# Performance work log

Measured on AMD Instinct MI355X. Metric: run time of the kernel, lower is better.

Reference implementation:

```python
import jax, jax.numpy as jnp
from jax import lax
import numpy as np

V, H = 512, 512


def gru_cell(x, h, Wih, Whh, bih, bhh):
    # PyTorch GRUCell: r,z,n gate order
    gi = x @ Wih.T + bih
    gh = h @ Whh.T + bhh
    ir, iz, inn = jnp.split(gi, 3, axis=-1)
    hr, hz, hn = jnp.split(gh, 3, axis=-1)
    r = jax.nn.sigmoid(ir + hr)
    z = jax.nn.sigmoid(iz + hz)
    n = jnp.tanh(inn + r * hn)
    return (1.0 - z) * n + z * h


def setup_inputs() -> dict:
    key = jax.random.key(0)
    ks = jax.random.split(key, 20)
    S, T, B = 200, 200, 256
    w = lambda k, shape: (jax.random.normal(k, shape, jnp.float32) * 0.05)
    inp = {
        "input_seq": jax.random.randint(ks[0], (S, B), 0, V),
        "input_len": jax.random.randint(ks[1], (B,), 1, S + 1),
        "target_seq": jax.random.randint(ks[2], (T, B), 0, V),
        "enc_embed": w(ks[3], (V, H)),
        "enc_Wih": w(ks[4], (3 * H, H)),
        "enc_Whh": w(ks[5], (3 * H, H)),
        "enc_bih": w(ks[6], (3 * H,)),
        "enc_bhh": w(ks[7], (3 * H,)),
        "att_W": w(ks[8], (H, H)),
        "att_b": w(ks[9], (H,)),
        "dec_embed": w(ks[10], (V, H)),
        "dec_Wih": w(ks[11], (3 * H, H)),
        "dec_Whh": w(ks[12], (3 * H, H)),
        "dec_bih": w(ks[13], (3 * H,)),
        "dec_bhh": w(ks[14], (3 * H,)),
        "mlp_W": w(ks[15], (H, 2 * H)),
        "mlp_b": w(ks[16], (H,)),
        "out_W": w(ks[17], (V, H)),
        "out_b": w(ks[18], (V,)),
    }
    return inp


def reference(input_seq, input_len, target_seq, enc_embed, enc_Wih, enc_Whh,
              enc_bih, enc_bhh, att_W, att_b, dec_embed, dec_Wih, dec_Whh,
              dec_bih, dec_bhh, mlp_W, mlp_b, out_W, out_b):
    S, B = input_seq.shape
    T = target_seq.shape[0]

    # ---- Encoder: length-masked GRU (equivalent to pack/pad) ----
    xs = enc_embed[input_seq]                              # (S,B,H)
    mask = jnp.arange(S)[:, None] < input_len[None, :]     # (S,B)
    h0 = jnp.zeros((B, H), xs.dtype)

    def estep(h, inp):
        x, m = inp
        m = m[:, None]
        hn = gru_cell(x, h, enc_Wih, enc_Whh, enc_bih, enc_bhh)
        h = jnp.where(m, hn, h)
        return h, jnp.where(m, h, 0.0)                     # padded outputs are zero

    h_enc, enc_out = lax.scan(estep, h0, (xs, mask))       # h_enc (B,H), enc_out (S,B,H)

    # ---- Decoder: teacher forcing (training path) ----
    dec_tokens = jnp.concatenate(
        [jnp.ones((1, B), target_seq.dtype), target_seq[:-1]], axis=0)  # start token 1
    dec_emb = dec_embed[dec_tokens]                        # (T,B,H)

    def dstep(h, emb_t):
        ah = jax.nn.relu(h @ att_W.T + att_b)              # (B,H)
        e = jnp.einsum('sbh,bh->bs', enc_out, ah)          # additive-style score
        att = jax.nn.softmax(e, axis=1)                    # (B,S)
        ctx = jnp.einsum('sbh,bs->bh', enc_out, att)       # (B,H)
        x = jnp.tanh(jnp.concatenate([emb_t, ctx], axis=1) @ mlp_W.T + mlp_b)
        hn = gru_cell(x, h, dec_Wih, dec_Whh, dec_bih, dec_bhh)
        dist = jax.nn.softmax(hn @ out_W.T + out_b, axis=1)
        return hn, dist

    _, dists = lax.scan(dstep, h_enc, dec_emb)             # (T,B,V)

    # ---- Loss: -log p[target] with clamp (== cal_loss) ----
    p = jnp.maximum(dists, 1e-10)
    tgt_p = jnp.take_along_axis(p, target_seq[:, :, None], axis=2)[..., 0]
    loss = jnp.mean(-jnp.log(tgt_p))

    # ---- Accuracy ----
    inference = jnp.argmax(dists, axis=-1)                 # (T,B)
    temacc = (inference == target_seq).astype(jnp.float32)
    all_acc = jnp.mean(temacc)
    acc = jnp.mean((jnp.sum(1.0 - temacc, axis=0) == 0).astype(jnp.float32))
    return inference.astype(jnp.float32), loss, acc, all_acc
```

## Files before the change

kernel.cpp:

```cpp
#include <hip/hip_runtime.h>
#include <math.h>

#define B 256
#define Hh 512
#define S 200
#define T 200
#define VOC 512
#define G3 1536
#define PAD 36

struct d4 { double x, y, z, w; };
__device__ __forceinline__ d4 tod4(const float4 a) {
    d4 r; r.x = a.x; r.y = a.y; r.z = a.z; r.w = a.w; return r;
}
__device__ __forceinline__ double dotd(const d4& a, const d4& b) {
    return a.x * b.x + a.y * b.y + a.z * b.z + a.w * b.w;
}
__device__ __forceinline__ double sigd(double x) { return 1.0 / (1.0 + exp(-x)); }

__global__ __launch_bounds__(256) void gemm_at(
    const float* __restrict__ A,
    const float* __restrict__ W, int ldw, int woff,
    const float* __restrict__ bias,
    float* __restrict__ C, int ldc)
{
    __shared__ float As[32][PAD];
    __shared__ float Ws[32][PAD];
    const int tid = threadIdx.x;
    const int tx = tid & 15, ty = tid >> 4;
    const int j0 = blockIdx.x * 32, m0 = blockIdx.y * 32;
    const int lr = tid >> 3, lc = (tid & 7) * 4;

    double acc00 = 0.0, acc01 = 0.0, acc10 = 0.0, acc11 = 0.0;

    for (int k0 = 0; k0 < 512; k0 += 32) {
        float4 av = *(const float4*)(A + (size_t)(m0 + lr) * 512 + k0 + lc);
        float4 wv = *(const float4*)(W + (size_t)(j0 + lr) * ldw + woff + k0 + lc);
        __syncthreads();
        *(float4*)&As[lr][lc] = av;
        *(float4*)&Ws[lr][lc] = wv;
        __syncthreads();
#pragma unroll
        for (int kk = 0; kk < 32; kk += 4) {
            d4 a0 = tod4(*(const float4*)&As[ty][kk]);
            d4 a1 = tod4(*(const float4*)&As[ty + 16][kk]);
            d4 b0 = tod4(*(const float4*)&Ws[tx][kk]);
            d4 b1 = tod4(*(const float4*)&Ws[tx + 16][kk]);
            acc00 += dotd(a0, b0);
            acc01 += dotd(a0, b1);
            acc10 += dotd(a1, b0);
            acc11 += dotd(a1, b1);
        }
    }
    const int ms[2] = { m0 + ty, m0 + ty + 16 };
    const int js[2] = { j0 + tx, j0 + tx + 16 };
    double accs[2][2] = { { acc00, acc01 }, { acc10, acc11 } };
#pragma unroll
    for (int mi = 0; mi < 2; ++mi)
#pragma unroll
        for (int ji = 0; ji < 2; ++ji) {
            int m = ms[mi], j = js[ji];
            C[(size_t)m * ldc + j] = (float)(accs[mi][ji] + (double)bias[j]);
        }
}

__global__ __launch_bounds__(512) void enc_step(
    const float* __restrict__ h_in, float* __restrict__ h_out,
    const float* __restrict__ gi_tab, const int* __restrict__ iseq,
    const int* __restrict__ ilen, const float* __restrict__ Whh,
    const float* __restrict__ bhh, int s, float* __restrict__ enc_out)
{
    __shared__ float Hs[32][68];
    __shared__ float Ws[48][68];
    const int tid = threadIdx.x;
    const int j_l = tid & 15, b_l = tid >> 4;
    const int j0 = blockIdx.x * 16, b0 = blockIdx.y * 32;
    const int j = j0 + j_l, b = b0 + b_l;

    int ml = 0;
    for (int i = 0; i < 32; ++i) ml = max(ml, ilen[b0 + i]);
    if (s >= ml) {
        h_out[(size_t)b * 512 + j] = h_in[(size_t)b * 512 + j];
        enc_out[((size_t)s * B + b) * 512 + j] = 0.f;
        return;
    }

    double ar = 0.0, az = 0.0, an = 0.0;
    for (int kt = 0; kt < 512; kt += 64) {
        __syncthreads();
        {
            int row = tid >> 4, c4 = (tid & 15) * 4;
            *(float4*)&Hs[row][c4] =
                *(const float4*)(h_in + (size_t)(b0 + row) * 512 + kt + c4);
            for (int idx = tid; idx < 768; idx += 512) {
                int r = idx >> 4, cc = (idx & 15) * 4;
                int g = r >> 4, jj = r & 15;
                *(float4*)&Ws[r][cc] =
                    *(const float4*)(Whh + (size_t)(g * 512 + j0 + jj) * 512 + kt + cc);
            }
        }
        __syncthreads();
#pragma unroll
        for (int kk = 0; kk < 64; kk += 4) {
            d4 hv = tod4(*(const float4*)&Hs[b_l][kk]);
            ar += dotd(hv, tod4(*(const float4*)&Ws[j_l][kk]));
            az += dotd(hv, tod4(*(const float4*)&Ws[16 + j_l][kk]));
            an += dotd(hv, tod4(*(const float4*)&Ws[32 + j_l][kk]));
        }
    }

    float hold = h_in[(size_t)b * 512 + j];
    float hnew = hold;
    if (s < ilen[b]) {
        int tok = iseq[s * B + b];
        const float* gi = gi_tab + (size_t)tok * G3;
        double r = sigd((double)gi[j] + ar + (double)bhh[j]);
        double z = sigd((double)gi[512 + j] + az + (double)bhh[512 + j]);
        double n = tanh((double)gi[1024 + j] + r * (an + (double)bhh[1024 + j]));
        hnew = (float)((1.0 - z) * n + z * (double)hold);
        enc_out[((size_t)s * B + b) * 512 + j] = hnew;
    } else {
        enc_out[((size_t)s * B + b) * 512 + j] = 0.f;
    }
    h_out[(size_t)b * 512 + j] = hnew;
}

__global__ __launch_bounds__(512) void proj(
    const float* __restrict__ h,
    const float* __restrict__ att_W, const float* __restrict__ att_b,
    const float* __restrict__ out_W, const float* __restrict__ out_b,
    float* __restrict__ ah, float* __restrict__ logits, int t)
{
    __shared__ float As[32][68];
    __shared__ float Ws[32][68];
    const int tid = threadIdx.x;
    const int tx = tid & 15, ty = tid >> 4;
    const int R0 = blockIdx.x * 32, m0 = blockIdx.y * 32;
    const bool is_att = (R0 < 512);
    if (is_att && t >= T) return;

    double a0 = 0.0, a1 = 0.0;
    for (int kt = 0; kt < 512; kt += 64) {
        __syncthreads();
        {
            int row = tid >> 4, c4 = (tid & 15) * 4;
            *(float4*)&As[row][c4] =
                *(const float4*)(h + (size_t)(m0 + row) * 512 + kt + c4);
            int R = R0 + row;
            const float* ws = is_att ? (att_W + (size_t)R * 512)
                                     : (out_W + (size_t)(R - 512) * 512);
            *(float4*)&Ws[row][c4] = *(const float4*)(ws + kt + c4);
        }
        __syncthreads();
#pragma unroll
        for (int kk = 0; kk < 64; kk += 4) {
            d4 av = tod4(*(const float4*)&As[ty][kk]);
            a0 += dotd(av, tod4(*(const float4*)&Ws[tx][kk]));
            a1 += dotd(av, tod4(*(const float4*)&Ws[16 + tx][kk]));
        }
    }

    const int m = m0 + ty;
    const int Ra = R0 + tx, Rb = R0 + tx + 16;
    if (is_att) {
        double v0 = a0 + (double)att_b[Ra]; if (v0 < 0.0) v0 = 0.0;
        double v1 = a1 + (double)att_b[Rb]; if (v1 < 0.0) v1 = 0.0;
        ah[(size_t)m * 512 + Ra] = (float)v0;
        ah[(size_t)m * 512 + Rb] = (float)v1;
    } else {
        logits[(size_t)m * 512 + (Ra - 512)] = (float)(a0 + (double)out_b[Ra - 512]);
        logits[(size_t)m * 512 + (Rb - 512)] = (float)(a1 + (double)out_b[Rb - 512]);
    }
}

__global__ __launch_bounds__(256) void attn_x_softmax(
    const float* __restrict__ enc_out, const float* __restrict__ ah,
    const float* __restrict__ mlp_W, const float* __restrict__ mlp_tab,
    const int* __restrict__ input_len, const int* __restrict__ target_seq,
    const float* __restrict__ logits, int t,
    float* __restrict__ xbuf, float* __restrict__ nll,
    float* __restrict__ inference)
{
    const int bid = blockIdx.x, tid = threadIdx.x;

    if (bid < B) {
        if (t >= T) return;
        __shared__ float scx[4][512];
        __shared__ double sml[8];
        __shared__ float ctxl[512];
        const int b = bid;
        const int wave = tid >> 6, lane = tid & 63;
        const int len = input_len[b];
        const float* ahb = ah + (size_t)b * 512;
        d4 aa1 = tod4(*(const float4*)(ahb + lane * 4));
        d4 aa2 = tod4(*(const float4*)(ahb + 256 + lane * 4));
        double m = -INFINITY, l = 0.0;
        d4 c1 = {0,0,0,0}, c2 = {0,0,0,0};
        for (int s = wave; s < len; s += 4) {
            const float* row = enc_out + ((size_t)s * B + b) * 512;
            d4 e1 = tod4(*(const float4*)(row + lane * 4));
            d4 e2 = tod4(*(const float4*)(row + 256 + lane * 4));
            double p = dotd(e1, aa1) + dotd(e2, aa2);
#pragma unroll
            for (int off = 32; off >= 1; off >>= 1) p += __shfl_xor(p, off, 64);
            double mn = fmax(m, p);
            double sc = (m == mn) ? 1.0 : exp(m - mn);
            double w = exp(p - mn);
            l = l * sc + w;
            c1.x = c1.x * sc + w * e1.x; c1.y = c1.y * sc + w * e1.y;
            c1.z = c1.z * sc + w * e1.z; c1.w = c1.w * sc + w * e1.w;
            c2.x = c2.x * sc + w * e2.x; c2.y = c2.y * sc + w * e2.y;
            c2.z = c2.z * sc + w * e2.z; c2.w = c2.w * sc + w * e2.w;
            m = mn;
        }
        if (lane == 0) { sml[wave] = m; sml[4 + wave] = l; }
        *(float4*)&scx[wave][lane * 4] =
            make_float4((float)c1.x, (float)c1.y, (float)c1.z, (float)c1.w);
        *(float4*)&scx[wave][256 + lane * 4] =
            make_float4((float)c2.x, (float)c2.y, (float)c2.z, (float)c2.w);
        __syncthreads();
        double M = fmax(fmax(sml[0], sml[1]), fmax(sml[2], sml[3]));
        if (len < S) M = fmax(M, 0.0);
        double w0 = exp(sml[0] - M), w1x = exp(sml[1] - M);
        double w2x = exp(sml[2] - M), w3 = exp(sml[3] - M);
        double L = sml[4] * w0 + sml[5] * w1x + sml[6] * w2x + sml[7] * w3
                 + (double)(S - len) * exp(0.0 - M);
        for (int jj = tid; jj < 512; jj += 256) {
            double v = (double)scx[0][jj] * w0 + (double)scx[1][jj] * w1x
                     + (double)scx[2][jj] * w2x + (double)scx[3][jj] * w3;
            ctxl[jj] = (float)(v / L);
        }
        __syncthreads();

        const int tok = (t == 0) ? 1 : target_seq[(t - 1) * B + b];
        const int q = tid & 3;
        const int rbase = tid >> 2;
#pragma unroll
        for (int pass = 0; pass < 8; ++pass) {
            const int jr = pass * 64 + rbase;
            const float* wr = mlp_W + (size_t)jr * 1024 + 512;
            double a = 0.0;
            for (int k = q * 4; k < 512; k += 16) {
                a += dotd(tod4(*(const float4*)&ctxl[k]),
                          tod4(*(const float4*)(wr + k)));
            }
            a += __shfl_xor(a, 1, 64);
            a += __shfl_xor(a, 2, 64);
            if (q == 0)
                xbuf[(size_t)b * 512 + jr] =
                    (float)tanh((double)mlp_tab[(size_t)tok * 512 + jr] + a);
        }
    } else {
        if (t < 1) return;
        __shared__ float red_f[256];
        __shared__ double red_d[256];
        __shared__ int red_i[256];
        const int sb = bid - B;
        const float* lg = logits + (size_t)sb * 512;
        const float l0 = lg[tid], l1 = lg[256 + tid];
        red_f[tid] = fmaxf(l0, l1);
        __syncthreads();
        for (int off = 128; off > 0; off >>= 1) {
            if (tid < off) red_f[tid] = fmaxf(red_f[tid], red_f[tid + off]);
            __syncthreads();
        }
        const double mx = (double)red_f[0];
        __syncthreads();
        const double e0 = exp((double)l0 - mx), e1 = exp((double)l1 - mx);
        red_d[tid] = e0 + e1;
        __syncthreads();
        for (int off = 128; off > 0; off >>= 1) {
            if (tid < off) red_d[tid] += red_d[tid + off];
            __syncthreads();
        }
        const double Z = red_d[0];
        __syncthreads();
        const float p0 = (float)(e0 / Z), p1 = (float)(e1 / Z);
        float v; int idx;
        if (p0 >= p1) { v = p0; idx = tid; } else { v = p1; idx = 256 + tid; }
        red_f[tid] = v; red_i[tid] = idx;
        __syncthreads();
        for (int off = 128; off > 0; off >>= 1) {
            if (tid < off) {
                float ov = red_f[tid + off]; int oi = red_i[tid + off];
                if (ov > red_f[tid] || (ov == red_f[tid] && oi < red_i[tid])) {
                    red_f[tid] = ov; red_i[tid] = oi;
                }
            }
            __syncthreads();
        }
        if (tid == 0) {
            int tg = target_seq[(t - 1) * B + sb];
            float pt = (float)(exp((double)lg[tg] - mx) / Z);
            pt = fmaxf(pt, 1e-10f);
            nll[(t - 1) * B + sb] = (float)(-log((double)pt));
            inference[(t - 1) * B + sb] = (float)red_i[0];
        }
    }
}

__global__ __launch_bounds__(256) void dec_gru(
    const float* __restrict__ x, const float* __restrict__ h_in,
    const float* __restrict__ Wih, const float* __restrict__ Whh,
    const float* __restrict__ bih, const float* __restrict__ bhh,
    float* __restrict__ h_out)
{
    __shared__ float Xs[16][36];
    __shared__ float Hs2[16][36];
    __shared__ float Wi[48][36];
    __shared__ float Wh[48][36];
    const int tid = threadIdx.x;
    const int j_l = tid & 15, b_l = tid >> 4;
    const int j0 = blockIdx.x * 16, b0 = blockIdx.y * 16;
    const int j = j0 + j_l, b = b0 + b_l;

    double air = 0, aiz = 0, ain = 0, ahr = 0, ahz = 0, ahn = 0;
    for (int kt = 0; kt < 512; kt += 32) {
        __syncthreads();
        for (int idx = tid; idx < 1024; idx += 256) {
            if (idx < 128) {
                int row = idx >> 3, c4 = (idx & 7) * 4;
                *(float4*)&Xs[row][c4] =
                    *(const float4*)(x + (size_t)(b0 + row) * 512 + kt + c4);
            } else if (idx < 256) {
                int w = idx - 128; int row = w >> 3, c4 = (w & 7) * 4;
                *(float4*)&Hs2[row][c4] =
                    *(const float4*)(h_in + (size_t)(b0 + row) * 512 + kt + c4);
            } else if (idx < 640) {
                int w = idx - 256; int row = w >> 3, c4 = (w & 7) * 4;
                int g = row >> 4, jj = row & 15;
                *(float4*)&Wi[row][c4] =
                    *(const float4*)(Wih + (size_t)(g * 512 + j0 + jj) * 512 + kt + c4);
            } else {
                int w = idx - 640; int row = w >> 3, c4 = (w & 7) * 4;
                int g = row >> 4, jj = row & 15;
                *(float4*)&Wh[row][c4] =
                    *(const float4*)(Whh + (size_t)(g * 512 + j0 + jj) * 512 + kt + c4);
            }
        }
        __syncthreads();
#pragma unroll
        for (int kk = 0; kk < 32; kk += 4) {
            d4 xv = tod4(*(const float4*)&Xs[b_l][kk]);
            d4 hv = tod4(*(const float4*)&Hs2[b_l][kk]);
            air += dotd(xv, tod4(*(const float4*)&Wi[j_l][kk]));
            aiz += dotd(xv, tod4(*(const float4*)&Wi[16 + j_l][kk]));
            ain += dotd(xv, tod4(*(const float4*)&Wi[32 + j_l][kk]));
            ahr += dotd(hv, tod4(*(const float4*)&Wh[j_l][kk]));
            ahz += dotd(hv, tod4(*(const float4*)&Wh[16 + j_l][kk]));
            ahn += dotd(hv, tod4(*(const float4*)&Wh[32 + j_l][kk]));
        }
    }

    double r = sigd(air + (double)bih[j] + ahr + (double)bhh[j]);
    double z = sigd(aiz + (double)bih[512 + j] + ahz + (double)bhh[512 + j]);
    double n = tanh(ain + (double)bih[1024 + j] + r * (ahn + (double)bhh[1024 + j]));
    float hold = h_in[(size_t)b * 512 + j];
    h_out[(size_t)b * 512 + j] = (float)((1.0 - z) * n + z * (double)hold);
}

__global__ __launch_bounds__(256) void finalize_k(
    const float* __restrict__ nll, const float* __restrict__ inference,
    const int* __restrict__ target, float* __restrict__ out3)
{
    const int tid = threadIdx.x;
    int wrong = 0;
    double match = 0.0;
    const int b = tid;
    for (int t = 0; t < T; ++t) {
        float inf = inference[t * B + b];
        float tg = (float)target[t * B + b];
        bool ok = (inf == tg);
        match += ok ? 1.0 : 0.0;
        wrong |= !ok;
    }
    double lsum = 0.0;
    for (int i = tid; i < T * B; i += 256) lsum += (double)nll[i];

    __shared__ double sl[256], sm_[256], sa[256];
    sl[tid] = lsum; sm_[tid] = match; sa[tid] = wrong ? 0.0 : 1.0;
    __syncthreads();
    for (int off = 128; off > 0; off >>= 1) {
        if (tid < off) {
            sl[tid] += sl[tid + off];
            sm_[tid] += sm_[tid + off];
            sa[tid] += sa[tid + off];
        }
        __syncthreads();
    }
    if (tid == 0) {
        out3[0] = (float)(sl[0] / (double)(T * B));
        out3[1] = (float)(sa[0] / (double)B);
        out3[2] = (float)(sm_[0] / (double)(T * B));
    }
}

extern "C" void kernel_launch(void* const* d_in, const int* in_sizes, int n_in,
                              void* d_out, int out_size, void* d_ws, size_t ws_size,
                              hipStream_t stream)
{
    const int*   input_seq  = (const int*)d_in[0];
    const int*   input_len  = (const int*)d_in[1];
    const int*   target_seq = (const int*)d_in[2];
    const float* enc_embed  = (const float*)d_in[3];
    const float* enc_Wih    = (const float*)d_in[4];
    const float* enc_Whh    = (const float*)d_in[5];
    const float* enc_bih    = (const float*)d_in[6];
    const float* enc_bhh    = (const float*)d_in[7];
    const float* att_W      = (const float*)d_in[8];
    const float* att_b      = (const float*)d_in[9];
    const float* dec_embed  = (const float*)d_in[10];
    const float* dec_Wih    = (const float*)d_in[11];
    const float* dec_Whh    = (const float*)d_in[12];
    const float* dec_bih    = (const float*)d_in[13];
    const float* dec_bhh    = (const float*)d_in[14];
    const float* mlp_W      = (const float*)d_in[15];
    const float* mlp_b      = (const float*)d_in[16];
    const float* out_W      = (const float*)d_in[17];
    const float* out_b      = (const float*)d_in[18];

    float* out = (float*)d_out;

    float* gi_tab  = (float*)d_ws;
    float* mlp_tab = gi_tab + (size_t)VOC * G3;
    float* h0      = mlp_tab + (size_t)VOC * Hh;
    float* h1      = h0 + (size_t)B * Hh;
    float* ahb     = h1 + (size_t)B * Hh;
    float* xb      = ahb + (size_t)B * Hh;
    float* lgb     = xb + (size_t)B * Hh;
    float* nllb    = lgb + (size_t)B * Hh;
    float* enc_out = nllb + (size_t)T * B;

    hipMemsetAsync(h0, 0, (size_t)B * Hh * sizeof(float), stream);

    gemm_at<<<dim3(48, 16), 256, 0, stream>>>(
        enc_embed, enc_Wih, 512, 0, enc_bih, gi_tab, G3);
    gemm_at<<<dim3(16, 16), 256, 0, stream>>>(
        dec_embed, mlp_W, 1024, 0, mlp_b, mlp_tab, Hh);

    for (int s = 0; s < S; ++s) {
        const float* hc = (s & 1) ? h1 : h0;
        float* hx = (s & 1) ? h0 : h1;
        enc_step<<<dim3(32, 8), 512, 0, stream>>>(
            hc, hx, gi_tab, input_seq, input_len, enc_Whh, enc_bhh, s, enc_out);
    }

    for (int t = 0; t <= T; ++t) {
        const float* hc = (t & 1) ? h1 : h0;
        float* hx = (t & 1) ? h0 : h1;
        proj<<<dim3(32, 8), 512, 0, stream>>>(
            hc, att_W, att_b, out_W, out_b, ahb, lgb, t);
        attn_x_softmax<<<dim3(2 * B), 256, 0, stream>>>(
            enc_out, ahb, mlp_W, mlp_tab, input_len, target_seq,
            lgb, t, xb, nllb, out);
        if (t < T) {
            dec_gru<<<dim3(32, 16), 256, 0, stream>>>(
                xb, hc, dec_Wih, dec_Whh, dec_bih, dec_bhh, hx);
        }
    }

    finalize_k<<<dim3(1), 256, 0, stream>>>(nllb, out, target_seq, out + (size_t)T * B);
}
```

Baseline: 33.33 ms.

## Move recurrent GEMMs to FP64 MFMA kernels with separate elementwise combine

Replaces the scalar double-precision dot-product kernels for the encoder step, projection and decoder GRU with a shared gemm64 kernel. It uses the 16x16x4 f64 MFMA instruction, probes the lane layout at runtime, and prefetches weight tiles through registers. The GEMM writes double partial sums to a workspace, and small combine kernels then apply biases and the gate nonlinearities. This should cut the per-step FP64 ALU cost, at the price of twice as many launches per step and an extra round trip of double intermediates through global memory.

```diff
diff --git a/kernel.cpp b/kernel.cpp
--- a/kernel.cpp
+++ b/kernel.cpp
@@ -17,6 +17,12 @@
     return a.x * b.x + a.y * b.y + a.z * b.z + a.w * b.w;
 }
 __device__ __forceinline__ double sigd(double x) { return 1.0 / (1.0 + exp(-x)); }
+
+typedef double f64x4 __attribute__((ext_vector_type(4)));
+
+__device__ __forceinline__ unsigned long long dbits(double v) {
+    return (unsigned long long)__double_as_longlong(v);
+}
 
 __global__ __launch_bounds__(256) void gemm_at(
     const float* __restrict__ A,
@@ -64,56 +70,123 @@
         }
 }
 
-__global__ __launch_bounds__(512) void enc_step(
+__global__ __launch_bounds__(128) void gemm64(
+    const float* __restrict__ A0, const float* __restrict__ A1,
+    const float* __restrict__ W0, const float* __restrict__ W1,
+    int split, int N, double* __restrict__ Csum,
+    const int* __restrict__ ilen, int s)
+{
+    const int n0 = blockIdx.x * 64;
+    const int m0 = blockIdx.y * 16;
+    if (ilen) {
+        int ml = 0;
+        for (int i = 0; i < 16; ++i) ml = max(ml, ilen[m0 + i]);
+        if (s >= ml) return;
+    }
+    __shared__ float As[16][516];
+    __shared__ float Ws[64][68];
+    const int tid = threadIdx.x;
+    const bool lo = (n0 < split);
+    const float* Ab = lo ? A0 : A1;
+    const float* Wb = lo ? W0 : W1;
+    const int nw = lo ? n0 : (n0 - split);
+
+    const int lane = tid & 63;
+    const int wv = tid >> 6;
+    const int lr = lane & 15;
+    const int g  = lane >> 4;
+
+    f64x4 zf = { 0.0, 0.0, 0.0, 0.0 };
+    f64x4 va = __builtin_amdgcn_mfma_f64_16x16x4f64(
+        (double)(1ULL << lane), 1.0, zf, 0, 0, 0);
+    const unsigned long long MM = 0xFFFFFFFFFFFFFULL;
+    const unsigned long long M0 = (1ULL << 36) | (1ULL << 20) | (1ULL << 4);
+    const int fam0 = __all(
+        ((dbits(va[0]) & MM) == M0) && ((dbits(va[1]) & MM) == M0) &&
+        ((dbits(va[2]) & MM) == M0) && ((dbits(va[3]) & MM) == M0));
+    const int am = fam0 ? (lane & 15) : (lane >> 2);
+    const int ak = fam0 ? (lane >> 4) : (lane & 3);
+    f64x4 vr = __builtin_amdgcn_mfma_f64_16x16x4f64(
+        (double)(1ULL << am), 1.0, zf, 0, 0, 0);
+
+#pragma unroll 4
+    for (int i = 0; i < 16; ++i) {
+        *(float4*)&As[i][tid * 4] =
+            *(const float4*)(Ab + (size_t)(m0 + i) * 512 + tid * 4);
+    }
+
+    float4 wreg[8];
+#pragma unroll
+    for (int i = 0; i < 8; ++i) {
+        int x4 = i * 128 + tid, row = x4 >> 4, c4 = (x4 & 15) * 4;
+        wreg[i] = *(const float4*)(Wb + (size_t)(nw + row) * 512 + c4);
+    }
+    __syncthreads();
+#pragma unroll
+    for (int i = 0; i < 8; ++i) {
+        int x4 = i * 128 + tid, row = x4 >> 4, c4 = (x4 & 15) * 4;
+        *(float4*)&Ws[row][c4] = wreg[i];
+    }
+    __syncthreads();
+
+    const int nl0 = wv * 32;
+    f64x4 c0 = { 0.0, 0.0, 0.0, 0.0 };
+    f64x4 c1 = { 0.0, 0.0, 0.0, 0.0 };
+
+    for (int k0 = 0; k0 < 512; k0 += 64) {
+        const bool more = (k0 + 64) < 512;
+        if (more) {
+#pragma unroll
+            for (int i = 0; i < 8; ++i) {
+                int x4 = i * 128 + tid, row = x4 >> 4, c4 = (x4 & 15) * 4;
+                wreg[i] = *(const float4*)(Wb + (size_t)(nw + row) * 512
+                                           + k0 + 64 + c4);
+            }
+        }
+#pragma unroll
+        for (int kk = 0; kk < 16; ++kk) {
+            double a  = (double)As[am][k0 + kk * 4 + ak];
+            double b0 = (double)Ws[nl0 + lr][kk * 4 + g];
+            double b1 = (double)Ws[nl0 + 16 + lr][kk * 4 + g];
+            c0 = __builtin_amdgcn_mfma_f64_16x16x4f64(a, b0, c0, 0, 0, 0);
+            c1 = __builtin_amdgcn_mfma_f64_16x16x4f64(a, b1, c1, 0, 0, 0);
+        }
+        __syncthreads();
+        if (more) {
+#pragma unroll
+            for (int i = 0; i < 8; ++i) {
+                int x4 = i * 128 + tid, row = x4 >> 4, c4 = (x4 & 15) * 4;
+                *(float4*)&Ws[row][c4] = wreg[i];
+            }
+            __syncthreads();
+        }
+    }
+
+#pragma unroll
+    for (int d = 0; d < 4; ++d) {
+        const int rowd = (int)((dbits(vr[d]) >> 52) & 0x7ff) - 1025;
+        const size_t m = (size_t)(m0 + rowd);
+        Csum[m * N + n0 + nl0 + lr]      = c0[d];
+        Csum[m * N + n0 + nl0 + 16 + lr] = c1[d];
+    }
+}
+
+__global__ __launch_bounds__(256) void enc_combine(
+    const double* __restrict__ Csum,
     const float* __restrict__ h_in, float* __restrict__ h_out,
     const float* __restrict__ gi_tab, const int* __restrict__ iseq,
-    const int* __restrict__ ilen, const float* __restrict__ Whh,
-    const float* __restrict__ bhh, int s, float* __restrict__ enc_out)
-{
-    __shared__ float Hs[32][68];
-    __shared__ float Ws[48][68];
-    const int tid = threadIdx.x;
-    const int j_l = tid & 15, b_l = tid >> 4;
-    const int j0 = blockIdx.x * 16, b0 = blockIdx.y * 32;
-    const int j = j0 + j_l, b = b0 + b_l;
-
-    int ml = 0;
-    for (int i = 0; i < 32; ++i) ml = max(ml, ilen[b0 + i]);
-    if (s >= ml) {
-        h_out[(size_t)b * 512 + j] = h_in[(size_t)b * 512 + j];
-        enc_out[((size_t)s * B + b) * 512 + j] = 0.f;
-        return;
-    }
-
-    double ar = 0.0, az = 0.0, an = 0.0;
-    for (int kt = 0; kt < 512; kt += 64) {
-        __syncthreads();
-        {
-            int row = tid >> 4, c4 = (tid & 15) * 4;
-            *(float4*)&Hs[row][c4] =
-                *(const float4*)(h_in + (size_t)(b0 + row) * 512 + kt + c4);
-            for (int idx = tid; idx < 768; idx += 512) {
-                int r = idx >> 4, cc = (idx & 15) * 4;
-                int g = r >> 4, jj = r & 15;
-                *(float4*)&Ws[r][cc] =
-                    *(const float4*)(Whh + (size_t)(g * 512 + j0 + jj) * 512 + kt + cc);
-            }
-        }
-        __syncthreads();
-#pragma unroll
-        for (int kk = 0; kk < 64; kk += 4) {
-            d4 hv = tod4(*(const float4*)&Hs[b_l][kk]);
-            ar += dotd(hv, tod4(*(const float4*)&Ws[j_l][kk]));
-            az += dotd(hv, tod4(*(const float4*)&Ws[16 + j_l][kk]));
-            an += dotd(hv, tod4(*(const float4*)&Ws[32 + j_l][kk]));
-        }
-    }
-
-    float hold = h_in[(size_t)b * 512 + j];
+    const int* __restrict__ ilen, const float* __restrict__ bhh,
+    int s, float* __restrict__ enc_out)
+{
+    const int idx = blockIdx.x * 256 + threadIdx.x;
+    const int b = idx >> 9, j = idx & 511;
+    const float hold = h_in[idx];
     float hnew = hold;
     if (s < ilen[b]) {
-        int tok = iseq[s * B + b];
+        const int tok = iseq[s * B + b];
         const float* gi = gi_tab + (size_t)tok * G3;
+        const double* Cb = Csum + (size_t)b * 1536;
+        double ar = Cb[j], az = Cb[512 + j], an = Cb[1024 + j];
         double r = sigd((double)gi[j] + ar + (double)bhh[j]);
         double z = sigd((double)gi[512 + j] + az + (double)bhh[512 + j]);
         double n = tanh((double)gi[1024 + j] + r * (an + (double)bhh[1024 + j]));
@@ -122,55 +195,41 @@
     } else {
         enc_out[((size_t)s * B + b) * 512 + j] = 0.f;
     }
-    h_out[(size_t)b * 512 + j] = hnew;
-}
-
-__global__ __launch_bounds__(512) void proj(
-    const float* __restrict__ h,
-    const float* __restrict__ att_W, const float* __restrict__ att_b,
-    const float* __restrict__ out_W, const float* __restrict__ out_b,
+    h_out[idx] = hnew;
+}
+
+__global__ __launch_bounds__(256) void proj_combine(
+    const double* __restrict__ Csum,
+    const float* __restrict__ att_b, const float* __restrict__ out_b,
     float* __restrict__ ah, float* __restrict__ logits, int t)
 {
-    __shared__ float As[32][68];
-    __shared__ float Ws[32][68];
-    const int tid = threadIdx.x;
-    const int tx = tid & 15, ty = tid >> 4;
-    const int R0 = blockIdx.x * 32, m0 = blockIdx.y * 32;
-    const bool is_att = (R0 < 512);
-    if (is_att && t >= T) return;
-
-    double a0 = 0.0, a1 = 0.0;
-    for (int kt = 0; kt < 512; kt += 64) {
-        __syncthreads();
-        {
-            int row = tid >> 4, c4 = (tid & 15) * 4;
-            *(float4*)&As[row][c4] =
-                *(const float4*)(h + (size_t)(m0 + row) * 512 + kt + c4);
-            int R = R0 + row;
-            const float* ws = is_att ? (att_W + (size_t)R * 512)
-                                     : (out_W + (size_t)(R - 512) * 512);
-            *(float4*)&Ws[row][c4] = *(const float4*)(ws + kt + c4);
-        }
-        __syncthreads();
-#pragma unroll
-        for (int kk = 0; kk < 64; kk += 4) {
-            d4 av = tod4(*(const float4*)&As[ty][kk]);
-            a0 += dotd(av, tod4(*(const float4*)&Ws[tx][kk]));
-            a1 += dotd(av, tod4(*(const float4*)&Ws[16 + tx][kk]));
-        }
-    }
-
-    const int m = m0 + ty;
-    const int Ra = R0 + tx, Rb = R0 + tx + 16;
-    if (is_att) {
-        double v0 = a0 + (double)att_b[Ra]; if (v0 < 0.0) v0 = 0.0;
-        double v1 = a1 + (double)att_b[Rb]; if (v1 < 0.0) v1 = 0.0;
-        ah[(size_t)m * 512 + Ra] = (float)v0;
-        ah[(size_t)m * 512 + Rb] = (float)v1;
+    const int idx = blockIdx.x * 256 + threadIdx.x;
+    const int m = idx >> 10, n = idx & 1023;
+    const double v = Csum[idx];
+    if (n < 512) {
+        if (t >= T) return;
+        double r = v + (double)att_b[n]; if (r < 0.0) r = 0.0;
+        ah[(size_t)m * 512 + n] = (float)r;
     } else {
-        logits[(size_t)m * 512 + (Ra - 512)] = (float)(a0 + (double)out_b[Ra - 512]);
-        logits[(size_t)m * 512 + (Rb - 512)] = (float)(a1 + (double)out_b[Rb - 512]);
-    }
+        logits[(size_t)m * 512 + (n - 512)] = (float)(v + (double)out_b[n - 512]);
+    }
+}
+
+__global__ __launch_bounds__(256) void dec_combine(
+    const double* __restrict__ Csum,
+    const float* __restrict__ bih, const float* __restrict__ bhh,
+    const float* __restrict__ h_in, float* __restrict__ h_out)
+{
+    const int idx = blockIdx.x * 256 + threadIdx.x;
+    const int b = idx >> 9, j = idx & 511;
+    const double* Cb = Csum + (size_t)b * 3072;
+    double air = Cb[j],        aiz = Cb[512 + j],  ain = Cb[1024 + j];
+    double ahr = Cb[1536 + j], ahz = Cb[2048 + j], ahn = Cb[2560 + j];
+    double r = sigd(air + (double)bih[j] + ahr + (double)bhh[j]);
+    double z = sigd(aiz + (double)bih[512 + j] + ahz + (double)bhh[512 + j]);
+    double n = tanh(ain + (double)bih[1024 + j] + r * (ahn + (double)bhh[1024 + j]));
+    const float hold = h_in[idx];
+    h_out[idx] = (float)((1.0 - z) * n + z * (double)hold);
 }
 
 __global__ __launch_bounds__(256) void attn_x_softmax(
@@ -297,66 +356,6 @@
             inference[(t - 1) * B + sb] = (float)red_i[0];
         }
     }
-}
-
-__global__ __launch_bounds__(256) void dec_gru(
-    const float* __restrict__ x, const float* __restrict__ h_in,
-    const float* __restrict__ Wih, const float* __restrict__ Whh,
-    const float* __restrict__ bih, const float* __restrict__ bhh,
-    float* __restrict__ h_out)
-{
-    __shared__ float Xs[16][36];
-    __shared__ float Hs2[16][36];
-    __shared__ float Wi[48][36];
-    __shared__ float Wh[48][36];
-    const int tid = threadIdx.x;
-    const int j_l = tid & 15, b_l = tid >> 4;
-    const int j0 = blockIdx.x * 16, b0 = blockIdx.y * 16;
-    const int j = j0 + j_l, b = b0 + b_l;
-
-    double air = 0, aiz = 0, ain = 0, ahr = 0, ahz = 0, ahn = 0;
-    for (int kt = 0; kt < 512; kt += 32) {
-        __syncthreads();
-        for (int idx = tid; idx < 1024; idx += 256) {
-            if (idx < 128) {
-                int row = idx >> 3, c4 = (idx & 7) * 4;
-                *(float4*)&Xs[row][c4] =
-                    *(const float4*)(x + (size_t)(b0 + row) * 512 + kt + c4);
-            } else if (idx < 256) {
-                int w = idx - 128; int row = w >> 3, c4 = (w & 7) * 4;
-                *(float4*)&Hs2[row][c4] =
-                    *(const float4*)(h_in + (size_t)(b0 + row) * 512 + kt + c4);
-            } else if (idx < 640) {
-                int w = idx - 256; int row = w >> 3, c4 = (w & 7) * 4;
-                int g = row >> 4, jj = row & 15;
-                *(float4*)&Wi[row][c4] =
-                    *(const float4*)(Wih + (size_t)(g * 512 + j0 + jj) * 512 + kt + c4);
-            } else {
-                int w = idx - 640; int row = w >> 3, c4 = (w & 7) * 4;
-                int g = row >> 4, jj = row & 15;
-                *(float4*)&Wh[row][c4] =
-                    *(const float4*)(Whh + (size_t)(g * 512 + j0 + jj) * 512 + kt + c4);
-            }
-        }
-        __syncthreads();
-#pragma unroll
-        for (int kk = 0; kk < 32; kk += 4) {
-            d4 xv = tod4(*(const float4*)&Xs[b_l][kk]);
-            d4 hv = tod4(*(const float4*)&Hs2[b_l][kk]);
-            air += dotd(xv, tod4(*(const float4*)&Wi[j_l][kk]));
-            aiz += dotd(xv, tod4(*(const float4*)&Wi[16 + j_l][kk]));
-            ain += dotd(xv, tod4(*(const float4*)&Wi[32 + j_l][kk]));
-            ahr += dotd(hv, tod4(*(const float4*)&Wh[j_l][kk]));
-            ahz += dotd(hv, tod4(*(const float4*)&Wh[16 + j_l][kk]));
-            ahn += dotd(hv, tod4(*(const float4*)&Wh[32 + j_l][kk]));
-        }
-    }
-
-    double r = sigd(air + (double)bih[j] + ahr + (double)bhh[j]);
-    double z = sigd(aiz + (double)bih[512 + j] + ahz + (double)bhh[512 + j]);
-    double n = tanh(ain + (double)bih[1024 + j] + r * (ahn + (double)bhh[1024 + j]));
-    float hold = h_in[(size_t)b * 512 + j];
-    h_out[(size_t)b * 512 + j] = (float)((1.0 - z) * n + z * (double)hold);
 }
 
 __global__ __launch_bounds__(256) void finalize_k(
@@ -430,6 +429,7 @@
     float* lgb     = xb + (size_t)B * Hh;
     float* nllb    = lgb + (size_t)B * Hh;
     float* enc_out = nllb + (size_t)T * B;
+    double* gsum   = (double*)(enc_out + (size_t)S * B * Hh);
 
     hipMemsetAsync(h0, 0, (size_t)B * Hh * sizeof(float), stream);
 
@@ -441,21 +441,27 @@
     for (int s = 0; s < S; ++s) {
         const float* hc = (s & 1) ? h1 : h0;
         float* hx = (s & 1) ? h0 : h1;
-        enc_step<<<dim3(32, 8), 512, 0, stream>>>(
-            hc, hx, gi_tab, input_seq, input_len, enc_Whh, enc_bhh, s, enc_out);
+        gemm64<<<dim3(24, 16), 128, 0, stream>>>(
+            hc, hc, enc_Whh, enc_Whh, 1536, 1536, gsum, input_len, s);
+        enc_combine<<<dim3(512), 256, 0, stream>>>(
+            gsum, hc, hx, gi_tab, input_seq, input_len, enc_bhh, s, enc_out);
     }
 
     for (int t = 0; t <= T; ++t) {
         const float* hc = (t & 1) ? h1 : h0;
         float* hx = (t & 1) ? h0 : h1;
-        proj<<<dim3(32, 8), 512, 0, stream>>>(
-            hc, att_W, att_b, out_W, out_b, ahb, lgb, t);
+        gemm64<<<dim3(16, 16), 128, 0, stream>>>(
+            hc, hc, att_W, out_W, 512, 1024, gsum, nullptr, 0);
+        proj_combine<<<dim3(1024), 256, 0, stream>>>(
+            gsum, att_b, out_b, ahb, lgb, t);
         attn_x_softmax<<<dim3(2 * B), 256, 0, stream>>>(
             enc_out, ahb, mlp_W, mlp_tab, input_len, target_seq,
             lgb, t, xb, nllb, out);
         if (t < T) {
-            dec_gru<<<dim3(32, 16), 256, 0, stream>>>(
-                xb, hc, dec_Wih, dec_Whh, dec_bih, dec_bhh, hx);
+            gemm64<<<dim3(48, 16), 128, 0, stream>>>(
+                xb, hc, dec_Wih, dec_Whh, 1536, 3072, gsum, nullptr, 0);
+            dec_combine<<<dim3(512), 256, 0, stream>>>(
+                gsum, dec_bih, dec_bhh, hc, hx);
         }
     }
 
```

Result: no change. 33.51 ms (+0.6%).

## Split attention into two-pass softmax context and separate tiled ctx-MLP GEMM

Applied to the files above, without the earlier changes.

The fused per-batch attention kernel, which did an online softmax and then a per-row matvec against mlp_W, is split in two. The first kernel stores scores in shared memory, does a block max and sum, and accumulates the context in a second pass over enc_out. A new shared-memory tiled GEMM then computes the ctx part of the MLP for all batches at once. This lets mlp_W be reused across batch rows instead of being reread by each of 256 blocks, at the cost of an extra launch, a second read of enc_out and a serial single-thread sum.

```diff
diff --git a/kernel.cpp b/kernel.cpp
--- a/kernel.cpp
+++ b/kernel.cpp
@@ -173,29 +173,26 @@
     }
 }
 
-__global__ __launch_bounds__(256) void attn_x_softmax(
+__global__ __launch_bounds__(256) void attn_ctx(
     const float* __restrict__ enc_out, const float* __restrict__ ah,
-    const float* __restrict__ mlp_W, const float* __restrict__ mlp_tab,
     const int* __restrict__ input_len, const int* __restrict__ target_seq,
     const float* __restrict__ logits, int t,
-    float* __restrict__ xbuf, float* __restrict__ nll,
+    float* __restrict__ ctxb, float* __restrict__ nll,
     float* __restrict__ inference)
 {
     const int bid = blockIdx.x, tid = threadIdx.x;
 
     if (bid < B) {
         if (t >= T) return;
-        __shared__ float scx[4][512];
-        __shared__ double sml[8];
-        __shared__ float ctxl[512];
+        __shared__ double e_w[200];
+        __shared__ double red[256];
         const int b = bid;
         const int wave = tid >> 6, lane = tid & 63;
         const int len = input_len[b];
         const float* ahb = ah + (size_t)b * 512;
         d4 aa1 = tod4(*(const float4*)(ahb + lane * 4));
         d4 aa2 = tod4(*(const float4*)(ahb + 256 + lane * 4));
-        double m = -INFINITY, l = 0.0;
-        d4 c1 = {0,0,0,0}, c2 = {0,0,0,0};
+
         for (int s = wave; s < len; s += 4) {
             const float* row = enc_out + ((size_t)s * B + b) * 512;
             d4 e1 = tod4(*(const float4*)(row + lane * 4));
@@ -203,53 +200,43 @@
             double p = dotd(e1, aa1) + dotd(e2, aa2);
 #pragma unroll
             for (int off = 32; off >= 1; off >>= 1) p += __shfl_xor(p, off, 64);
-            double mn = fmax(m, p);
-            double sc = (m == mn) ? 1.0 : exp(m - mn);
-            double w = exp(p - mn);
-            l = l * sc + w;
-            c1.x = c1.x * sc + w * e1.x; c1.y = c1.y * sc + w * e1.y;
-            c1.z = c1.z * sc + w * e1.z; c1.w = c1.w * sc + w * e1.w;
-            c2.x = c2.x * sc + w * e2.x; c2.y = c2.y * sc + w * e2.y;
-            c2.z = c2.z * sc + w * e2.z; c2.w = c2.w * sc + w * e2.w;
-            m = mn;
-        }
-        if (lane == 0) { sml[wave] = m; sml[4 + wave] = l; }
-        *(float4*)&scx[wave][lane * 4] =
-            make_float4((float)c1.x, (float)c1.y, (float)c1.z, (float)c1.w);
-        *(float4*)&scx[wave][256 + lane * 4] =
-            make_float4((float)c2.x, (float)c2.y, (float)c2.z, (float)c2.w);
-        __syncthreads();
-        double M = fmax(fmax(sml[0], sml[1]), fmax(sml[2], sml[3]));
+            if (lane == 0) e_w[s] = p;
+        }
+        __syncthreads();
+
+        double mloc = -INFINITY;
+        for (int s2 = tid; s2 < len; s2 += 256) mloc = fmax(mloc, e_w[s2]);
+        red[tid] = mloc;
+        __syncthreads();
+        for (int off = 128; off > 0; off >>= 1) {
+            if (tid < off) red[tid] = fmax(red[tid], red[tid + off]);
+            __syncthreads();
+        }
+        double M = red[0];
         if (len < S) M = fmax(M, 0.0);
-        double w0 = exp(sml[0] - M), w1x = exp(sml[1] - M);
-        double w2x = exp(sml[2] - M), w3 = exp(sml[3] - M);
-        double L = sml[4] * w0 + sml[5] * w1x + sml[6] * w2x + sml[7] * w3
-                 + (double)(S - len) * exp(0.0 - M);
-        for (int jj = tid; jj < 512; jj += 256) {
-            double v = (double)scx[0][jj] * w0 + (double)scx[1][jj] * w1x
-                     + (double)scx[2][jj] * w2x + (double)scx[3][jj] * w3;
-            ctxl[jj] = (float)(v / L);
-        }
-        __syncthreads();
-
-        const int tok = (t == 0) ? 1 : target_seq[(t - 1) * B + b];
-        const int q = tid & 3;
-        const int rbase = tid >> 2;
-#pragma unroll
-        for (int pass = 0; pass < 8; ++pass) {
-            const int jr = pass * 64 + rbase;
-            const float* wr = mlp_W + (size_t)jr * 1024 + 512;
-            double a = 0.0;
-            for (int k = q * 4; k < 512; k += 16) {
-                a += dotd(tod4(*(const float4*)&ctxl[k]),
-                          tod4(*(const float4*)(wr + k)));
-            }
-            a += __shfl_xor(a, 1, 64);
-            a += __shfl_xor(a, 2, 64);
-            if (q == 0)
-                xbuf[(size_t)b * 512 + jr] =
-                    (float)tanh((double)mlp_tab[(size_t)tok * 512 + jr] + a);
-        }
+        __syncthreads();
+
+        if (tid < len) e_w[tid] = exp(e_w[tid] - M);
+        __syncthreads();
+
+        if (tid == 0) {
+            double acc = 0.0;
+            for (int s2 = 0; s2 < len; ++s2) acc += e_w[s2];
+            acc += (double)(S - len) * exp(0.0 - M);
+            red[0] = acc;
+        }
+        __syncthreads();
+        const double L = red[0];
+
+        double acc0 = 0.0, acc1 = 0.0;
+        for (int s2 = 0; s2 < len; ++s2) {
+            const float* row = enc_out + ((size_t)s2 * B + b) * 512;
+            const double w = e_w[s2];
+            acc0 += w * (double)row[tid];
+            acc1 += w * (double)row[tid + 256];
+        }
+        ctxb[(size_t)b * 512 + tid]       = (float)(acc0 / L);
+        ctxb[(size_t)b * 512 + tid + 256] = (float)(acc1 / L);
     } else {
         if (t < 1) return;
         __shared__ float red_f[256];
@@ -297,6 +284,45 @@
             inference[(t - 1) * B + sb] = (float)red_i[0];
         }
     }
+}
+
+__global__ __launch_bounds__(512) void xgemm(
+    const float* __restrict__ ctxb, const float* __restrict__ mlp_W,
+    const float* __restrict__ mlp_tab, const int* __restrict__ target_seq,
+    int t, float* __restrict__ xb)
+{
+    __shared__ float As[32][68];
+    __shared__ float Ws[32][68];
+    const int tid = threadIdx.x;
+    const int tx = tid & 15, ty = tid >> 4;
+    const int j0 = blockIdx.x * 32, m0 = blockIdx.y * 32;
+
+    double a0 = 0.0, a1 = 0.0;
+    for (int kt = 0; kt < 512; kt += 64) {
+        __syncthreads();
+        {
+            int row = tid >> 4, c4 = (tid & 15) * 4;
+            *(float4*)&As[row][c4] =
+                *(const float4*)(ctxb + (size_t)(m0 + row) * 512 + kt + c4);
+            *(float4*)&Ws[row][c4] =
+                *(const float4*)(mlp_W + (size_t)(j0 + row) * 1024 + 512 + kt + c4);
+        }
+        __syncthreads();
+#pragma unroll
+        for (int kk = 0; kk < 64; kk += 4) {
+            d4 av = tod4(*(const float4*)&As[ty][kk]);
+            a0 += dotd(av, tod4(*(const float4*)&Ws[tx][kk]));
+            a1 += dotd(av, tod4(*(const float4*)&Ws[16 + tx][kk]));
+        }
+    }
+
+    const int m = m0 + ty;
+    const int tok = (t == 0) ? 1 : target_seq[(t - 1) * B + m];
+    const int ja = j0 + tx, jb = j0 + tx + 16;
+    xb[(size_t)m * 512 + ja] =
+        (float)tanh((double)mlp_tab[(size_t)tok * 512 + ja] + a0);
+    xb[(size_t)m * 512 + jb] =
+        (float)tanh((double)mlp_tab[(size_t)tok * 512 + jb] + a1);
 }
 
 __global__ __launch_bounds__(256) void dec_gru(
@@ -430,6 +456,7 @@
     float* lgb     = xb + (size_t)B * Hh;
     float* nllb    = lgb + (size_t)B * Hh;
     float* enc_out = nllb + (size_t)T * B;
+    float* ctxb    = enc_out + (size_t)S * B * Hh;
 
     hipMemsetAsync(h0, 0, (size_t)B * Hh * sizeof(float), stream);
 
@@ -450,10 +477,11 @@
         float* hx = (t & 1) ? h0 : h1;
         proj<<<dim3(32, 8), 512, 0, stream>>>(
             hc, att_W, att_b, out_W, out_b, ahb, lgb, t);
-        attn_x_softmax<<<dim3(2 * B), 256, 0, stream>>>(
-            enc_out, ahb, mlp_W, mlp_tab, input_len, target_seq,
-            lgb, t, xb, nllb, out);
+        attn_ctx<<<dim3(2 * B), 256, 0, stream>>>(
+            enc_out, ahb, input_len, target_seq, lgb, t, ctxb, nllb, out);
         if (t < T) {
+            xgemm<<<dim3(16, 8), 512, 0, stream>>>(
+                ctxb, mlp_W, mlp_tab, target_seq, t, xb);
             dec_gru<<<dim3(32, 16), 256, 0, stream>>>(
                 xb, hc, dec_Wih, dec_Whh, dec_bih, dec_bhh, hx);
         }
```

New measurement: 34.87 ms. +4.6%, slower.

## Register-prefetch next K tile and shrink tiles in GRU and projection kernels

Applied to the files above, without the earlier changes.

Rewrites the encoder step, projection, and decoder GRU kernels to prefetch the next 64-wide K tile into registers while computing on the current shared-memory tile. Tiles shrink to 16x16 with 256-thread blocks, giving more blocks per launch (e.g. 512 for the encoder and 1024 for the projection). The decoder GRU K tile grows from 32 to 64. The aim is to hide global-load latency and raise occupancy on these latency-bound per-timestep launches, at the cost of more register pressure and less reuse per block.

```diff
diff --git a/kernel.cpp b/kernel.cpp
--- a/kernel.cpp
+++ b/kernel.cpp
@@ -64,42 +64,59 @@
         }
 }
 
-__global__ __launch_bounds__(512) void enc_step(
+__global__ __launch_bounds__(256) void enc_step2(
     const float* __restrict__ h_in, float* __restrict__ h_out,
     const float* __restrict__ gi_tab, const int* __restrict__ iseq,
     const int* __restrict__ ilen, const float* __restrict__ Whh,
     const float* __restrict__ bhh, int s, float* __restrict__ enc_out)
 {
-    __shared__ float Hs[32][68];
+    __shared__ float Hs[16][68];
     __shared__ float Ws[48][68];
     const int tid = threadIdx.x;
     const int j_l = tid & 15, b_l = tid >> 4;
-    const int j0 = blockIdx.x * 16, b0 = blockIdx.y * 32;
+    const int j0 = blockIdx.x * 16, b0 = blockIdx.y * 16;
     const int j = j0 + j_l, b = b0 + b_l;
 
     int ml = 0;
-    for (int i = 0; i < 32; ++i) ml = max(ml, ilen[b0 + i]);
+    for (int i = 0; i < 16; ++i) ml = max(ml, ilen[b0 + i]);
     if (s >= ml) {
         h_out[(size_t)b * 512 + j] = h_in[(size_t)b * 512 + j];
         enc_out[((size_t)s * B + b) * 512 + j] = 0.f;
         return;
     }
 
+    const int srow = (tid >> 4) & 63;
+    float4 pre[4];
+#pragma unroll
+    for (int i = 0; i < 4; ++i) {
+        int x4 = i * 256 + tid, row = x4 >> 4, c4 = (x4 & 15) * 4;
+        const float* p = (row < 16)
+            ? (h_in + (size_t)(b0 + row) * 512 + c4)
+            : (Whh + (size_t)(((row - 16) >> 4) * 512 + j0 + ((row - 16) & 15)) * 512 + c4);
+        pre[i] = *(const float4*)p;
+    }
+    (void)srow;
+
     double ar = 0.0, az = 0.0, an = 0.0;
     for (int kt = 0; kt < 512; kt += 64) {
         __syncthreads();
-        {
-            int row = tid >> 4, c4 = (tid & 15) * 4;
-            *(float4*)&Hs[row][c4] =
-                *(const float4*)(h_in + (size_t)(b0 + row) * 512 + kt + c4);
-            for (int idx = tid; idx < 768; idx += 512) {
-                int r = idx >> 4, cc = (idx & 15) * 4;
-                int g = r >> 4, jj = r & 15;
-                *(float4*)&Ws[r][cc] =
-                    *(const float4*)(Whh + (size_t)(g * 512 + j0 + jj) * 512 + kt + cc);
+#pragma unroll
+        for (int i = 0; i < 4; ++i) {
+            int x4 = i * 256 + tid, row = x4 >> 4, c4 = (x4 & 15) * 4;
+            if (row < 16) *(float4*)&Hs[row][c4] = pre[i];
+            else          *(float4*)&Ws[row - 16][c4] = pre[i];
+        }
+        __syncthreads();
+        if (kt + 64 < 512) {
+#pragma unroll
+            for (int i = 0; i < 4; ++i) {
+                int x4 = i * 256 + tid, row = x4 >> 4, c4 = (x4 & 15) * 4;
+                const float* p = (row < 16)
+                    ? (h_in + (size_t)(b0 + row) * 512 + kt + 64 + c4)
+                    : (Whh + (size_t)(((row - 16) >> 4) * 512 + j0 + ((row - 16) & 15)) * 512 + kt + 64 + c4);
+                pre[i] = *(const float4*)p;
             }
         }
-        __syncthreads();
 #pragma unroll
         for (int kk = 0; kk < 64; kk += 4) {
             d4 hv = tod4(*(const float4*)&Hs[b_l][kk]);
@@ -125,51 +142,72 @@
     h_out[(size_t)b * 512 + j] = hnew;
 }
 
-__global__ __launch_bounds__(512) void proj(
+__global__ __launch_bounds__(256) void proj2(
     const float* __restrict__ h,
     const float* __restrict__ att_W, const float* __restrict__ att_b,
     const float* __restrict__ out_W, const float* __restrict__ out_b,
     float* __restrict__ ah, float* __restrict__ logits, int t)
 {
-    __shared__ float As[32][68];
-    __shared__ float Ws[32][68];
+    __shared__ float As[16][68];
+    __shared__ float Ws[16][68];
     const int tid = threadIdx.x;
     const int tx = tid & 15, ty = tid >> 4;
-    const int R0 = blockIdx.x * 32, m0 = blockIdx.y * 32;
-    const bool is_att = (R0 < 512);
+    const int Rb0 = blockIdx.x * 16, m0 = blockIdx.y * 16;
+    const bool is_att = (Rb0 < 512);
     if (is_att && t >= T) return;
 
-    double a0 = 0.0, a1 = 0.0;
+    float4 pre[2];
+#pragma unroll
+    for (int i = 0; i < 2; ++i) {
+        int x4 = i * 256 + tid, row = x4 >> 4, c4 = (x4 & 15) * 4;
+        const float* p;
+        if (row < 16) p = h + (size_t)(m0 + row) * 512 + c4;
+        else {
+            int R = Rb0 + row - 16;
+            p = is_att ? (att_W + (size_t)R * 512 + c4)
+                       : (out_W + (size_t)(R - 512) * 512 + c4);
+        }
+        pre[i] = *(const float4*)p;
+    }
+
+    double a0 = 0.0;
     for (int kt = 0; kt < 512; kt += 64) {
         __syncthreads();
-        {
-            int row = tid >> 4, c4 = (tid & 15) * 4;
-            *(float4*)&As[row][c4] =
-                *(const float4*)(h + (size_t)(m0 + row) * 512 + kt + c4);
-            int R = R0 + row;
-            const float* ws = is_att ? (att_W + (size_t)R * 512)
-                                     : (out_W + (size_t)(R - 512) * 512);
-            *(float4*)&Ws[row][c4] = *(const float4*)(ws + kt + c4);
-        }
-        __syncthreads();
+#pragma unroll
+        for (int i = 0; i < 2; ++i) {
+            int x4 = i * 256 + tid, row = x4 >> 4, c4 = (x4 & 15) * 4;
+            if (row < 16) *(float4*)&As[row][c4] = pre[i];
+            else          *(float4*)&Ws[row - 16][c4] = pre[i];
+        }
+        __syncthreads();
+        if (kt + 64 < 512) {
+#pragma unroll
+            for (int i = 0; i < 2; ++i) {
+                int x4 = i * 256 + tid, row = x4 >> 4, c4 = (x4 & 15) * 4;
+                const float* p;
+                if (row < 16) p = h + (size_t)(m0 + row) * 512 + kt + 64 + c4;
+                else {
+                    int R = Rb0 + row - 16;
+                    p = is_att ? (att_W + (size_t)R * 512 + kt + 64 + c4)
+                               : (out_W + (size_t)(R - 512) * 512 + kt + 64 + c4);
+                }
+                pre[i] = *(const float4*)p;
+            }
+        }
 #pragma unroll
         for (int kk = 0; kk < 64; kk += 4) {
-            d4 av = tod4(*(const float4*)&As[ty][kk]);
-            a0 += dotd(av, tod4(*(const float4*)&Ws[tx][kk]));
-            a1 += dotd(av, tod4(*(const float4*)&Ws[16 + tx][kk]));
+            a0 += dotd(tod4(*(const float4*)&As[ty][kk]),
+                       tod4(*(const float4*)&Ws[tx][kk]));
         }
     }
 
     const int m = m0 + ty;
-    const int Ra = R0 + tx, Rb = R0 + tx + 16;
+    const int R = Rb0 + tx;
     if (is_att) {
-        double v0 = a0 + (double)att_b[Ra]; if (v0 < 0.0) v0 = 0.0;
-        double v1 = a1 + (double)att_b[Rb]; if (v1 < 0.0) v1 = 0.0;
-        ah[(size_t)m * 512 + Ra] = (float)v0;
-        ah[(size_t)m * 512 + Rb] = (float)v1;
+        double v0 = a0 + (double)att_b[R]; if (v0 < 0.0) v0 = 0.0;
+        ah[(size_t)m * 512 + R] = (float)v0;
     } else {
-        logits[(size_t)m * 512 + (Ra - 512)] = (float)(a0 + (double)out_b[Ra - 512]);
-        logits[(size_t)m * 512 + (Rb - 512)] = (float)(a1 + (double)out_b[Rb - 512]);
+        logits[(size_t)m * 512 + (R - 512)] = (float)(a0 + (double)out_b[R - 512]);
     }
 }
 
@@ -299,48 +337,69 @@
     }
 }
 
-__global__ __launch_bounds__(256) void dec_gru(
+__global__ __launch_bounds__(256) void dec_gru2(
     const float* __restrict__ x, const float* __restrict__ h_in,
     const float* __restrict__ Wih, const float* __restrict__ Whh,
     const float* __restrict__ bih, const float* __restrict__ bhh,
     float* __restrict__ h_out)
 {
-    __shared__ float Xs[16][36];
-    __shared__ float Hs2[16][36];
-    __shared__ float Wi[48][36];
-    __shared__ float Wh[48][36];
+    __shared__ float Xs[16][68];
+    __shared__ float Hs2[16][68];
+    __shared__ float Wi[48][68];
+    __shared__ float Wh[48][68];
     const int tid = threadIdx.x;
     const int j_l = tid & 15, b_l = tid >> 4;
     const int j0 = blockIdx.x * 16, b0 = blockIdx.y * 16;
     const int j = j0 + j_l, b = b0 + b_l;
 
+    float4 pre[8];
+#pragma unroll
+    for (int i = 0; i < 8; ++i) {
+        int x4 = i * 256 + tid, row = x4 >> 4, c4 = (x4 & 15) * 4;
+        const float* p;
+        if (row < 16)      p = x + (size_t)(b0 + row) * 512 + c4;
+        else if (row < 32) p = h_in + (size_t)(b0 + row - 16) * 512 + c4;
+        else if (row < 80) {
+            int r = row - 32;
+            p = Wih + (size_t)((r >> 4) * 512 + j0 + (r & 15)) * 512 + c4;
+        } else {
+            int r = row - 80;
+            p = Whh + (size_t)((r >> 4) * 512 + j0 + (r & 15)) * 512 + c4;
+        }
+        pre[i] = *(const float4*)p;
+    }
+
     double air = 0, aiz = 0, ain = 0, ahr = 0, ahz = 0, ahn = 0;
-    for (int kt = 0; kt < 512; kt += 32) {
-        __syncthreads();
-        for (int idx = tid; idx < 1024; idx += 256) {
-            if (idx < 128) {
-                int row = idx >> 3, c4 = (idx & 7) * 4;
-                *(float4*)&Xs[row][c4] =
-                    *(const float4*)(x + (size_t)(b0 + row) * 512 + kt + c4);
-            } else if (idx < 256) {
-                int w = idx - 128; int row = w >> 3, c4 = (w & 7) * 4;
-                *(float4*)&Hs2[row][c4] =
-                    *(const float4*)(h_in + (size_t)(b0 + row) * 512 + kt + c4);
-            } else if (idx < 640) {
-                int w = idx - 256; int row = w >> 3, c4 = (w & 7) * 4;
-                int g = row >> 4, jj = row & 15;
-                *(float4*)&Wi[row][c4] =
-                    *(const float4*)(Wih + (size_t)(g * 512 + j0 + jj) * 512 + kt + c4);
-            } else {
-                int w = idx - 640; int row = w >> 3, c4 = (w & 7) * 4;
-                int g = row >> 4, jj = row & 15;
-                *(float4*)&Wh[row][c4] =
-                    *(const float4*)(Whh + (size_t)(g * 512 + j0 + jj) * 512 + kt + c4);
+    for (int kt = 0; kt < 512; kt += 64) {
+        __syncthreads();
+#pragma unroll
+        for (int i = 0; i < 8; ++i) {
+            int x4 = i * 256 + tid, row = x4 >> 4, c4 = (x4 & 15) * 4;
+            if (row < 16)      *(float4*)&Xs[row][c4] = pre[i];
+            else if (row < 32) *(float4*)&Hs2[row - 16][c4] = pre[i];
+            else if (row < 80) *(float4*)&Wi[row - 32][c4] = pre[i];
+            else               *(float4*)&Wh[row - 80][c4] = pre[i];
+        }
+        __syncthreads();
+        if (kt + 64 < 512) {
+#pragma unroll
+            for (int i = 0; i < 8; ++i) {
+                int x4 = i * 256 + tid, row = x4 >> 4, c4 = (x4 & 15) * 4;
+                const float* p;
+                if (row < 16)      p = x + (size_t)(b0 + row) * 512 + kt + 64 + c4;
+                else if (row < 32) p = h_in + (size_t)(b0 + row - 16) * 512 + kt + 64 + c4;
+                else if (row < 80) {
+                    int r = row - 32;
+                    p = Wih + (size_t)((r >> 4) * 512 + j0 + (r & 15)) * 512 + kt + 64 + c4;
+                } else {
+                    int r = row - 80;
+                    p = Whh + (size_t)((r >> 4) * 512 + j0 + (r & 15)) * 512 + kt + 64 + c4;
+                }
+                pre[i] = *(const float4*)p;
             }
         }
-        __syncthreads();
-#pragma unroll
-        for (int kk = 0; kk < 32; kk += 4) {
+#pragma unroll
+        for (int kk = 0; kk < 64; kk += 4) {
             d4 xv = tod4(*(const float4*)&Xs[b_l][kk]);
             d4 hv = tod4(*(const float4*)&Hs2[b_l][kk]);
             air += dotd(xv, tod4(*(const float4*)&Wi[j_l][kk]));
@@ -441,20 +500,20 @@
     for (int s = 0; s < S; ++s) {
         const float* hc = (s & 1) ? h1 : h0;
         float* hx = (s & 1) ? h0 : h1;
-        enc_step<<<dim3(32, 8), 512, 0, stream>>>(
+        enc_step2<<<dim3(32, 16), 256, 0, stream>>>(
             hc, hx, gi_tab, input_seq, input_len, enc_Whh, enc_bhh, s, enc_out);
     }
 
     for (int t = 0; t <= T; ++t) {
         const float* hc = (t & 1) ? h1 : h0;
         float* hx = (t & 1) ? h0 : h1;
-        proj<<<dim3(32, 8), 512, 0, stream>>>(
+        proj2<<<dim3(64, 16), 256, 0, stream>>>(
             hc, att_W, att_b, out_W, out_b, ahb, lgb, t);
         attn_x_softmax<<<dim3(2 * B), 256, 0, stream>>>(
             enc_out, ahb, mlp_W, mlp_tab, input_len, target_seq,
             lgb, t, xb, nllb, out);
         if (t < T) {
-            dec_gru<<<dim3(32, 16), 256, 0, stream>>>(
+            dec_gru2<<<dim3(32, 16), 256, 0, stream>>>(
                 xb, hc, dec_Wih, dec_Whh, dec_bih, dec_bhh, hx);
         }
     }
```

Result: slower. 39.69 ms (+19.1%).
